# Optimization experiments

Hardware: AMD Instinct MI355X
Metric: run time of the kernel (lower is better)

The kernel has to match this reference:

```python
import jax, jax.numpy as jnp
import numpy as np

B = 32768
T = 1024  # num_time_bins


def setup_inputs() -> dict:
    key = jax.random.key(0)
    k1, k2, k3, k4 = jax.random.split(key, 4)
    hazard_values = jax.random.uniform(k1, (B, T), dtype=jnp.float32)
    labels_Y = jax.random.uniform(k2, (B,), dtype=jnp.float32) * T
    # nn.Linear(T, T): weight [T, T] (out, in), bias [T]
    lim = 1.0 / np.sqrt(T)
    W = jax.random.uniform(k3, (T, T), minval=-lim, maxval=lim, dtype=jnp.float32)
    b = jax.random.uniform(k4, (T,), minval=-lim, maxval=lim, dtype=jnp.float32)
    return {"hazard_values": hazard_values, "labels_Y": labels_Y, "W": W, "b": b}


def reference(hazard_values, labels_Y, W, b):
    # linear + sigmoid + argmax -> per-row truncation position
    logits = hazard_values @ W.T + b                       # [B, T]
    trunc_pos = jnp.argmax(jax.nn.sigmoid(logits), axis=1, keepdims=True)  # [B, 1] int
    # survival curve
    S = jnp.cumprod(1.0 - hazard_values, axis=1)           # [B, T]
    # vectorized truncation decay: for t >= p, multiply by exp(-(t - p))
    t = jnp.arange(T)[None, :]                             # [1, T]
    decay = jnp.where(t >= trunc_pos,
                      jnp.exp(-(t - trunc_pos).astype(S.dtype)),
                      jnp.ones((), S.dtype))
    S = S * decay
    # MSE between argmax position and labels (original prints; we skip prints)
    p = trunc_pos[:, 0].astype(jnp.float32)
    truncation_loss = jnp.mean((p - labels_Y) ** 2)
    return trunc_pos, S, truncation_loss
```

## Files before the change

kernel.cpp:

```cpp
#include <hip/hip_runtime.h>

#define B_ROWS 32768
#define T_BINS 1024

typedef __attribute__((ext_vector_type(8))) _Float16 half8;
typedef __attribute__((ext_vector_type(4))) float floatx4;

__device__ __forceinline__ unsigned long long pack_max(float v, int col) {
    unsigned x = __float_as_uint(v);
    x = (x & 0x80000000u) ? ~x : (x | 0x80000000u);
    return ((unsigned long long)x << 32) | (unsigned)(~col);
}

__device__ __forceinline__ void async16h(const _Float16* g, _Float16* l) {
    __builtin_amdgcn_global_load_lds(
        (const __attribute__((address_space(1))) unsigned int*)g,
        (__attribute__((address_space(3))) unsigned int*)l,
        16, 0, 0);
}

__global__ __launch_bounds__(256) void tof16_kernel(
    const float* __restrict__ src, _Float16* __restrict__ dst, int n4)
{
    int idx = blockIdx.x * 256 + threadIdx.x;
    if (idx >= n4) return;
    float4 x = ((const float4*)src)[idx];
    union { _Float16 h[4]; ushort4 u; } cv;
    cv.h[0] = (_Float16)x.x;
    cv.h[1] = (_Float16)x.y;
    cv.h[2] = (_Float16)x.z;
    cv.h[3] = (_Float16)x.w;
    ((ushort4*)dst)[idx] = cv.u;
}

__global__ __launch_bounds__(256, 2) void mega_kernel(
    const float* __restrict__ A, const _Float16* __restrict__ Wh,
    const float* __restrict__ bias, const float* __restrict__ labels,
    float* __restrict__ out_trunc, float* __restrict__ out_S,
    float* __restrict__ loss_acc)
{
    __shared__ _Float16 sA[2][64 * 64];
    __shared__ _Float16 sW[2][256 * 64];

    const int tid  = threadIdx.x;
    const int lane = tid & 63;
    const int wc   = tid >> 6;
    const int by   = blockIdx.x;

    const int arow = tid >> 2;
    const int ac   = tid & 3;
    const int x8a  = (arow ^ (arow >> 3)) & 7;
    const int sAw0 = arow * 64 + (((ac * 2) ^ x8a) * 8);
    const int sAw1 = arow * 64 + (((ac * 2 + 1) ^ x8a) * 8);
    const float* Abase = A + (size_t)(by * 64 + arow) * T_BINS + ac * 16;

    const int l3   = lane >> 3;
    const int wsl  = lane & 7;

    const int l15  = lane & 15;
    const int hi   = lane >> 4;
    const int xc   = (l15 & 7) ^ (l15 >> 3);

    float run_best[4][4];
    int   run_col[4][4];
#pragma unroll
    for (int i = 0; i < 4; ++i)
#pragma unroll
        for (int r = 0; r < 4; ++r) { run_best[i][r] = -3.4e38f; run_col[i][r] = 0; }

    {
        float4 f0 = *(const float4*)(Abase + 0);
        float4 f1 = *(const float4*)(Abase + 4);
        float4 f2 = *(const float4*)(Abase + 8);
        float4 f3 = *(const float4*)(Abase + 12);
        half8 h0, h1;
        h0[0] = (_Float16)f0.x; h0[1] = (_Float16)f0.y; h0[2] = (_Float16)f0.z; h0[3] = (_Float16)f0.w;
        h0[4] = (_Float16)f1.x; h0[5] = (_Float16)f1.y; h0[6] = (_Float16)f1.z; h0[7] = (_Float16)f1.w;
        h1[0] = (_Float16)f2.x; h1[1] = (_Float16)f2.y; h1[2] = (_Float16)f2.z; h1[3] = (_Float16)f2.w;
        h1[4] = (_Float16)f3.x; h1[5] = (_Float16)f3.y; h1[6] = (_Float16)f3.z; h1[7] = (_Float16)f3.w;
        *(half8*)&sA[0][sAw0] = h0;
        *(half8*)&sA[0][sAw1] = h1;
    }
#pragma unroll
    for (int r = 0; r < 8; ++r)
        async16h(Wh + (size_t)(wc * 64 + r * 8 + l3) * T_BINS + ((wsl ^ l3 ^ r) * 8),
                 &sW[0][(wc * 64 + r * 8) * 64]);
    float4 pa0 = *(const float4*)(Abase + 64);
    float4 pa1 = *(const float4*)(Abase + 68);
    float4 pa2 = *(const float4*)(Abase + 72);
    float4 pa3 = *(const float4*)(Abase + 76);
    __syncthreads();

    int n = 0;
    for (int bx = 0; bx < 4; ++bx) {
        const int colbase = bx * 256 + wc * 64 + l15;
        float bj[4];
#pragma unroll
        for (int j = 0; j < 4; ++j) bj[j] = bias[colbase + j * 16];

        floatx4 acc[4][4];
#pragma unroll
        for (int i = 0; i < 4; ++i)
#pragma unroll
            for (int j = 0; j < 4; ++j) acc[i][j] = (floatx4){0.f, 0.f, 0.f, 0.f};

        for (int t = 0; t < 16; ++t, ++n) {
            const int cur = n & 1;
            const int nxt = cur ^ 1;

            if (n < 63) {
                const int m   = n + 1;
                const int bxn = m >> 4;
                const int k0n = (m & 15) * 64;

#pragma unroll
                for (int r = 0; r < 8; ++r)
                    async16h(Wh + (size_t)(bxn * 256 + wc * 64 + r * 8 + l3) * T_BINS
                                + k0n + ((wsl ^ l3 ^ r) * 8),
                             &sW[nxt][(wc * 64 + r * 8) * 64]);

                const int kq = ((n + 2) & 15) * 64;
                float4 qa0 = *(const float4*)(Abase + kq + 0);
                float4 qa1 = *(const float4*)(Abase + kq + 4);
                float4 qa2 = *(const float4*)(Abase + kq + 8);
                float4 qa3 = *(const float4*)(Abase + kq + 12);

                {
                    half8 h0, h1;
                    h0[0] = (_Float16)pa0.x; h0[1] = (_Float16)pa0.y; h0[2] = (_Float16)pa0.z; h0[3] = (_Float16)pa0.w;
                    h0[4] = (_Float16)pa1.x; h0[5] = (_Float16)pa1.y; h0[6] = (_Float16)pa1.z; h0[7] = (_Float16)pa1.w;
                    h1[0] = (_Float16)pa2.x; h1[1] = (_Float16)pa2.y; h1[2] = (_Float16)pa2.z; h1[3] = (_Float16)pa2.w;
                    h1[4] = (_Float16)pa3.x; h1[5] = (_Float16)pa3.y; h1[6] = (_Float16)pa3.z; h1[7] = (_Float16)pa3.w;
                    *(half8*)&sA[nxt][sAw0] = h0;
                    *(half8*)&sA[nxt][sAw1] = h1;
                }
                pa0 = qa0; pa1 = qa1; pa2 = qa2; pa3 = qa3;
            }

#pragma unroll
            for (int g = 0; g < 2; ++g) {
                half8 ah[4], whf[4];
#pragma unroll
                for (int i = 0; i < 4; ++i)
                    ah[i] = *(const half8*)&sA[cur][(i * 16 + l15) * 64
                                                    + (((g * 4 + hi) ^ xc ^ (i * 2)) * 8)];
#pragma unroll
                for (int j = 0; j < 4; ++j)
                    whf[j] = *(const half8*)&sW[cur][(wc * 64 + j * 16 + l15) * 64
                                                     + (((g * 4 + hi) ^ xc ^ (j * 2)) * 8)];
#pragma unroll
                for (int i = 0; i < 4; ++i)
#pragma unroll
                    for (int j = 0; j < 4; ++j)
                        acc[i][j] = __builtin_amdgcn_mfma_f32_16x16x32_f16(ah[i], whf[j], acc[i][j], 0, 0, 0);
            }

            __syncthreads();
        }

#pragma unroll
        for (int i = 0; i < 4; ++i)
#pragma unroll
            for (int r = 0; r < 4; ++r)
#pragma unroll
                for (int j = 0; j < 4; ++j) {
                    float v = acc[i][j][r] + bj[j];
                    if (v > run_best[i][r]) { run_best[i][r] = v; run_col[i][r] = colbase + j * 16; }
                }
    }

    unsigned long long (*cand)[64] = reinterpret_cast<unsigned long long (*)[64]>(&sA[0][0]);
    float* trunc_s = reinterpret_cast<float*>(&sA[0][0]) + 512;

#pragma unroll
    for (int i = 0; i < 4; ++i)
#pragma unroll
        for (int r = 0; r < 4; ++r) {
            float best = run_best[i][r];
            int   bc   = run_col[i][r];
#pragma unroll
            for (int off = 8; off >= 1; off >>= 1) {
                float ov = __shfl_xor(best, off, 64);
                int   oc = __shfl_xor(bc, off, 64);
                if (ov > best || (ov == best && oc < bc)) { best = ov; bc = oc; }
            }
            if ((lane & 15) == 0)
                cand[wc][i * 16 + (lane >> 4) * 4 + r] = pack_max(best, bc);
        }
    __syncthreads();

    if (tid < 64) {
        unsigned long long m01 = cand[0][tid] > cand[1][tid] ? cand[0][tid] : cand[1][tid];
        unsigned long long m23 = cand[2][tid] > cand[3][tid] ? cand[2][tid] : cand[3][tid];
        unsigned long long mm = m01 > m23 ? m01 : m23;
        unsigned col = ~(unsigned)mm;
        float p = (float)col;
        int rowG = by * 64 + tid;
        out_trunc[rowG] = p;
        trunc_s[tid] = p;
        float d = p - labels[rowG];
        float term = d * d * (1.0f / (float)B_ROWS);
#pragma unroll
        for (int off = 32; off >= 1; off >>= 1)
            term += __shfl_down(term, off, 64);
        if (tid == 0) atomicAdd(loss_acc, term);
    }
    __syncthreads();

    for (int rr = 0; rr < 16; ++rr) {
        int row  = wc * 16 + rr;
        int rowG = by * 64 + row;
        const float* Hrow = A + (size_t)rowG * T_BINS + lane * 16;
        float4 h0 = *(const float4*)(Hrow + 0);
        float4 h1 = *(const float4*)(Hrow + 4);
        float4 h2 = *(const float4*)(Hrow + 8);
        float4 h3 = *(const float4*)(Hrow + 12);
        float hv[16] = {h0.x, h0.y, h0.z, h0.w, h1.x, h1.y, h1.z, h1.w,
                        h2.x, h2.y, h2.z, h2.w, h3.x, h3.y, h3.z, h3.w};
        float vprod[16];
        float run = 1.f;
#pragma unroll
        for (int j = 0; j < 16; ++j) { run *= (1.f - hv[j]); vprod[j] = run; }
        float x = run;
#pragma unroll
        for (int off = 1; off < 64; off <<= 1) {
            float o = __shfl_up(x, off, 64);
            if (lane >= off) x *= o;
        }
        float pre = __shfl_up(x, 1, 64);
        if (lane == 0) pre = 1.f;

        int p  = (int)trunc_s[row];
        int t0 = lane * 16;
        float sv[16];
#pragma unroll
        for (int j = 0; j < 16; ++j) {
            float s = pre * vprod[j];
            int t = t0 + j;
            if (t >= p) s *= __expf((float)(p - t));
            sv[j] = s;
        }
        float* Srow = out_S + (size_t)rowG * T_BINS + lane * 16;
        *(float4*)(Srow + 0)  = (float4){sv[0],  sv[1],  sv[2],  sv[3]};
        *(float4*)(Srow + 4)  = (float4){sv[4],  sv[5],  sv[6],  sv[7]};
        *(float4*)(Srow + 8)  = (float4){sv[8],  sv[9],  sv[10], sv[11]};
        *(float4*)(Srow + 12) = (float4){sv[12], sv[13], sv[14], sv[15]};
    }
}

#define BMf 64
#define BKf 16
#define LDSS (BMf + 4)
__global__ __launch_bounds__(256) void gemm_argmax_fp32(
    const float* __restrict__ A, const float* __restrict__ W,
    const float* __restrict__ bias, unsigned long long* __restrict__ rec)
{
    __shared__ float As[BKf][LDSS];
    __shared__ float Ws[BKf][LDSS];
    const int tid = threadIdx.x;
    const int tx = tid & 15, ty = tid >> 4;
    const int bx = blockIdx.x, by = blockIdx.y;
    const int ar = tid >> 2, ak = (tid & 3) << 2;
    const float* Arow = A + (size_t)(by * BMf + ar) * T_BINS + ak;
    const float* Wrow = W + (size_t)(bx * BMf + ar) * T_BINS + ak;
    float acc[4][4];
#pragma unroll
    for (int i = 0; i < 4; ++i)
#pragma unroll
        for (int j = 0; j < 4; ++j) acc[i][j] = 0.f;
    for (int k0 = 0; k0 < T_BINS; k0 += BKf) {
        float4 av = *(const float4*)(Arow + k0);
        float4 wvv = *(const float4*)(Wrow + k0);
        As[ak + 0][ar] = av.x; As[ak + 1][ar] = av.y; As[ak + 2][ar] = av.z; As[ak + 3][ar] = av.w;
        Ws[ak + 0][ar] = wvv.x; Ws[ak + 1][ar] = wvv.y; Ws[ak + 2][ar] = wvv.z; Ws[ak + 3][ar] = wvv.w;
        __syncthreads();
#pragma unroll
        for (int k = 0; k < BKf; ++k) {
            float4 a4 = *(const float4*)&As[k][ty * 4];
            float4 w4 = *(const float4*)&Ws[k][tx * 4];
            float aa[4] = {a4.x, a4.y, a4.z, a4.w};
            float ww[4] = {w4.x, w4.y, w4.z, w4.w};
#pragma unroll
            for (int i = 0; i < 4; ++i)
#pragma unroll
                for (int j = 0; j < 4; ++j) acc[i][j] = fmaf(aa[i], ww[j], acc[i][j]);
        }
        __syncthreads();
    }
    const int colBase = bx * BMf + tx * 4;
    float bv[4];
#pragma unroll
    for (int j = 0; j < 4; ++j) bv[j] = bias[colBase + j];
#pragma unroll
    for (int i = 0; i < 4; ++i) {
        float best = acc[i][0] + bv[0];
        int bc = colBase;
#pragma unroll
        for (int j = 1; j < 4; ++j) {
            float v = acc[i][j] + bv[j];
            if (v > best) { best = v; bc = colBase + j; }
        }
#pragma unroll
        for (int off = 8; off >= 1; off >>= 1) {
            float ov = __shfl_xor(best, off, 64);
            int oc = __shfl_xor(bc, off, 64);
            if (ov > best || (ov == best && oc < bc)) { best = ov; bc = oc; }
        }
        if (tx == 0) atomicMax(&rec[by * BMf + ty * 4 + i], pack_max(best, bc));
    }
}

__global__ __launch_bounds__(256) void finalize_kernel(
    const unsigned long long* __restrict__ rec, const float* __restrict__ labels,
    float* __restrict__ out_trunc, float* __restrict__ loss_acc)
{
    int i = blockIdx.x * 256 + threadIdx.x;
    unsigned col = ~(unsigned)(rec[i] & 0xFFFFFFFFull);
    float p = (float)col;
    out_trunc[i] = p;
    float d = p - labels[i];
    float term = d * d * (1.0f / (float)B_ROWS);
#pragma unroll
    for (int off = 32; off >= 1; off >>= 1)
        term += __shfl_down(term, off, 64);
    __shared__ float partials[4];
    int lane = threadIdx.x & 63, wv = threadIdx.x >> 6;
    if (lane == 0) partials[wv] = term;
    __syncthreads();
    if (threadIdx.x == 0)
        atomicAdd(loss_acc, partials[0] + partials[1] + partials[2] + partials[3]);
}

__global__ __launch_bounds__(256) void scan_kernel_f32(
    const float* __restrict__ H, const float* __restrict__ trunc_f,
    float* __restrict__ Sout)
{
    const int row = blockIdx.x;
    const int tid = threadIdx.x;
    const int lane = tid & 63;
    const int wv = tid >> 6;
    const float4 h = *(const float4*)(H + (size_t)row * T_BINS + tid * 4);
    float l0 = 1.f - h.x;
    float l1 = l0 * (1.f - h.y);
    float l2 = l1 * (1.f - h.z);
    float l3 = l2 * (1.f - h.w);
    float x = l3;
#pragma unroll
    for (int off = 1; off < 64; off <<= 1) {
        float o = __shfl_up(x, off, 64);
        if (lane >= off) x *= o;
    }
    float ex = __shfl_up(x, 1, 64);
    if (lane == 0) ex = 1.f;
    __shared__ float wtot[4];
    if (lane == 63) wtot[wv] = x;
    __syncthreads();
    float wpre = 1.f;
#pragma unroll
    for (int w = 0; w < 3; ++w)
        if (w < wv) wpre *= wtot[w];
    float pre = wpre * ex;
    int p = (int)trunc_f[row];
    int t0 = tid * 4;
    float sv[4] = {pre * l0, pre * l1, pre * l2, pre * l3};
#pragma unroll
    for (int j = 0; j < 4; ++j) {
        int t = t0 + j;
        if (t >= p) sv[j] *= __expf((float)(p - t));
    }
    float4 s4 = {sv[0], sv[1], sv[2], sv[3]};
    *(float4*)(Sout + (size_t)row * T_BINS + tid * 4) = s4;
}

extern "C" void kernel_launch(void* const* d_in, const int* in_sizes, int n_in,
                              void* d_out, int out_size, void* d_ws, size_t ws_size,
                              hipStream_t stream)
{
    const float* hazard = (const float*)d_in[0];
    const float* labels = (const float*)d_in[1];
    const float* W      = (const float*)d_in[2];
    const float* bias   = (const float*)d_in[3];

    float* out       = (float*)d_out;
    float* out_trunc = out;
    float* out_S     = out + B_ROWS;
    float* out_loss  = out + B_ROWS + (size_t)B_ROWS * T_BINS;

    hipMemsetAsync(out_loss, 0, sizeof(float), stream);

    const size_t NW = (size_t)T_BINS * T_BINS;
    if (ws_size >= NW * sizeof(_Float16)) {
        _Float16* Wh = (_Float16*)d_ws;
        tof16_kernel<<<(int)(NW / 4 / 256), 256, 0, stream>>>(W, Wh, (int)(NW / 4));
        mega_kernel<<<B_ROWS / 64, 256, 0, stream>>>(
            hazard, Wh, bias, labels, out_trunc, out_S, out_loss);
    } else {
        unsigned long long* rec = (unsigned long long*)out_S;
        hipMemsetAsync(rec, 0, (size_t)B_ROWS * sizeof(unsigned long long), stream);
        dim3 ggrid(T_BINS / BMf, B_ROWS / BMf);
        gemm_argmax_fp32<<<ggrid, 256, 0, stream>>>(hazard, W, bias, rec);
        finalize_kernel<<<B_ROWS / 256, 256, 0, stream>>>(rec, labels, out_trunc, out_loss);
        scan_kernel_f32<<<B_ROWS, 256, 0, stream>>>(hazard, out_trunc, out_S);
    }
}
```

Measured before the change: 354.1 us.

## Split mega kernel work across 8 waves per block instead of 4

Doubles the block to 512 threads so each wave computes a 64x32 output sub-tile instead of 64x64. The A and W staging loads are redistributed across the 8 waves, with the swizzle adjusted by an extra per-wave XOR term. The argmax candidate merge now reduces over 8 waves, and the scan/decay epilogue handles 8 rows per wave. The aim is more waves in flight and fewer accumulator registers per thread to hide latency, at the cost of re-reading the A fragments from LDS twice as often per MFMA.

```diff
diff --git a/kernel.cpp b/kernel.cpp
--- a/kernel.cpp
+++ b/kernel.cpp
@@ -33,7 +33,7 @@
     ((ushort4*)dst)[idx] = cv.u;
 }
 
-__global__ __launch_bounds__(256, 2) void mega_kernel(
+__global__ __launch_bounds__(512, 4) void mega_kernel(
     const float* __restrict__ A, const _Float16* __restrict__ Wh,
     const float* __restrict__ bias, const float* __restrict__ labels,
     float* __restrict__ out_trunc, float* __restrict__ out_S,
@@ -44,22 +44,23 @@
 
     const int tid  = threadIdx.x;
     const int lane = tid & 63;
-    const int wc   = tid >> 6;
+    const int w    = tid >> 6;
     const int by   = blockIdx.x;
 
-    const int arow = tid >> 2;
-    const int ac   = tid & 3;
+    const int arow = tid >> 3;
+    const int c8   = tid & 7;
     const int x8a  = (arow ^ (arow >> 3)) & 7;
-    const int sAw0 = arow * 64 + (((ac * 2) ^ x8a) * 8);
-    const int sAw1 = arow * 64 + (((ac * 2 + 1) ^ x8a) * 8);
-    const float* Abase = A + (size_t)(by * 64 + arow) * T_BINS + ac * 16;
-
-    const int l3   = lane >> 3;
-    const int wsl  = lane & 7;
-
-    const int l15  = lane & 15;
-    const int hi   = lane >> 4;
-    const int xc   = (l15 & 7) ^ (l15 >> 3);
+    const int asc  = c8 ^ x8a;
+    const float* Abase = A + (size_t)(by * 64 + arow) * T_BINS + asc * 8;
+    const int sAw  = arow * 64 + c8 * 8;
+
+    const int l3  = lane >> 3;
+    const int wsl = lane & 7;
+    const int w4  = (w & 1) * 4;
+
+    const int l15 = lane & 15;
+    const int hi  = lane >> 4;
+    const int xc  = (l15 & 7) ^ (l15 >> 3);
 
     float run_best[4][4];
     int   run_col[4][4];
@@ -71,38 +72,31 @@
     {
         float4 f0 = *(const float4*)(Abase + 0);
         float4 f1 = *(const float4*)(Abase + 4);
-        float4 f2 = *(const float4*)(Abase + 8);
-        float4 f3 = *(const float4*)(Abase + 12);
-        half8 h0, h1;
-        h0[0] = (_Float16)f0.x; h0[1] = (_Float16)f0.y; h0[2] = (_Float16)f0.z; h0[3] = (_Float16)f0.w;
-        h0[4] = (_Float16)f1.x; h0[5] = (_Float16)f1.y; h0[6] = (_Float16)f1.z; h0[7] = (_Float16)f1.w;
-        h1[0] = (_Float16)f2.x; h1[1] = (_Float16)f2.y; h1[2] = (_Float16)f2.z; h1[3] = (_Float16)f2.w;
-        h1[4] = (_Float16)f3.x; h1[5] = (_Float16)f3.y; h1[6] = (_Float16)f3.z; h1[7] = (_Float16)f3.w;
-        *(half8*)&sA[0][sAw0] = h0;
-        *(half8*)&sA[0][sAw1] = h1;
-    }
-#pragma unroll
-    for (int r = 0; r < 8; ++r)
-        async16h(Wh + (size_t)(wc * 64 + r * 8 + l3) * T_BINS + ((wsl ^ l3 ^ r) * 8),
-                 &sW[0][(wc * 64 + r * 8) * 64]);
+        half8 hv;
+        hv[0] = (_Float16)f0.x; hv[1] = (_Float16)f0.y; hv[2] = (_Float16)f0.z; hv[3] = (_Float16)f0.w;
+        hv[4] = (_Float16)f1.x; hv[5] = (_Float16)f1.y; hv[6] = (_Float16)f1.z; hv[7] = (_Float16)f1.w;
+        *(half8*)&sA[0][sAw] = hv;
+    }
+#pragma unroll
+    for (int r = 0; r < 4; ++r)
+        async16h(Wh + (size_t)(w * 32 + r * 8 + l3) * T_BINS + ((wsl ^ l3 ^ w4 ^ r) * 8),
+                 &sW[0][(w * 32 + r * 8) * 64]);
     float4 pa0 = *(const float4*)(Abase + 64);
     float4 pa1 = *(const float4*)(Abase + 68);
-    float4 pa2 = *(const float4*)(Abase + 72);
-    float4 pa3 = *(const float4*)(Abase + 76);
     __syncthreads();
 
     int n = 0;
     for (int bx = 0; bx < 4; ++bx) {
-        const int colbase = bx * 256 + wc * 64 + l15;
-        float bj[4];
-#pragma unroll
-        for (int j = 0; j < 4; ++j) bj[j] = bias[colbase + j * 16];
-
-        floatx4 acc[4][4];
+        const int colbase = bx * 256 + w * 32 + l15;
+        float bj[2];
+        bj[0] = bias[colbase];
+        bj[1] = bias[colbase + 16];
+
+        floatx4 acc[4][2];
 #pragma unroll
         for (int i = 0; i < 4; ++i)
 #pragma unroll
-            for (int j = 0; j < 4; ++j) acc[i][j] = (floatx4){0.f, 0.f, 0.f, 0.f};
+            for (int j = 0; j < 2; ++j) acc[i][j] = (floatx4){0.f, 0.f, 0.f, 0.f};
 
         for (int t = 0; t < 16; ++t, ++n) {
             const int cur = n & 1;
@@ -114,44 +108,41 @@
                 const int k0n = (m & 15) * 64;
 
 #pragma unroll
-                for (int r = 0; r < 8; ++r)
-                    async16h(Wh + (size_t)(bxn * 256 + wc * 64 + r * 8 + l3) * T_BINS
-                                + k0n + ((wsl ^ l3 ^ r) * 8),
-                             &sW[nxt][(wc * 64 + r * 8) * 64]);
+                for (int r = 0; r < 4; ++r)
+                    async16h(Wh + (size_t)(bxn * 256 + w * 32 + r * 8 + l3) * T_BINS
+                                + k0n + ((wsl ^ l3 ^ w4 ^ r) * 8),
+                             &sW[nxt][(w * 32 + r * 8) * 64]);
 
                 const int kq = ((n + 2) & 15) * 64;
                 float4 qa0 = *(const float4*)(Abase + kq + 0);
                 float4 qa1 = *(const float4*)(Abase + kq + 4);
-                float4 qa2 = *(const float4*)(Abase + kq + 8);
-                float4 qa3 = *(const float4*)(Abase + kq + 12);
 
                 {
-                    half8 h0, h1;
-                    h0[0] = (_Float16)pa0.x; h0[1] = (_Float16)pa0.y; h0[2] = (_Float16)pa0.z; h0[3] = (_Float16)pa0.w;
-                    h0[4] = (_Float16)pa1.x; h0[5] = (_Float16)pa1.y; h0[6] = (_Float16)pa1.z; h0[7] = (_Float16)pa1.w;
-                    h1[0] = (_Float16)pa2.x; h1[1] = (_Float16)pa2.y; h1[2] = (_Float16)pa2.z; h1[3] = (_Float16)pa2.w;
-                    h1[4] = (_Float16)pa3.x; h1[5] = (_Float16)pa3.y; h1[6] = (_Float16)pa3.z; h1[7] = (_Float16)pa3.w;
-                    *(half8*)&sA[nxt][sAw0] = h0;
-                    *(half8*)&sA[nxt][sAw1] = h1;
+                    half8 hv;
+                    hv[0] = (_Float16)pa0.x; hv[1] = (_Float16)pa0.y;
+                    hv[2] = (_Float16)pa0.z; hv[3] = (_Float16)pa0.w;
+                    hv[4] = (_Float16)pa1.x; hv[5] = (_Float16)pa1.y;
+                    hv[6] = (_Float16)pa1.z; hv[7] = (_Float16)pa1.w;
+                    *(half8*)&sA[nxt][sAw] = hv;
                 }
-                pa0 = qa0; pa1 = qa1; pa2 = qa2; pa3 = qa3;
+                pa0 = qa0; pa1 = qa1;
             }
 
 #pragma unroll
             for (int g = 0; g < 2; ++g) {
-                half8 ah[4], whf[4];
+                half8 ah[4], whf[2];
 #pragma unroll
                 for (int i = 0; i < 4; ++i)
                     ah[i] = *(const half8*)&sA[cur][(i * 16 + l15) * 64
                                                     + (((g * 4 + hi) ^ xc ^ (i * 2)) * 8)];
 #pragma unroll
-                for (int j = 0; j < 4; ++j)
-                    whf[j] = *(const half8*)&sW[cur][(wc * 64 + j * 16 + l15) * 64
-                                                     + (((g * 4 + hi) ^ xc ^ (j * 2)) * 8)];
+                for (int j = 0; j < 2; ++j)
+                    whf[j] = *(const half8*)&sW[cur][(w * 32 + j * 16 + l15) * 64
+                                                     + (((g * 4 + hi) ^ xc ^ (j * 2) ^ w4) * 8)];
 #pragma unroll
                 for (int i = 0; i < 4; ++i)
 #pragma unroll
-                    for (int j = 0; j < 4; ++j)
+                    for (int j = 0; j < 2; ++j)
                         acc[i][j] = __builtin_amdgcn_mfma_f32_16x16x32_f16(ah[i], whf[j], acc[i][j], 0, 0, 0);
             }
 
@@ -163,14 +154,14 @@
 #pragma unroll
             for (int r = 0; r < 4; ++r)
 #pragma unroll
-                for (int j = 0; j < 4; ++j) {
+                for (int j = 0; j < 2; ++j) {
                     float v = acc[i][j][r] + bj[j];
                     if (v > run_best[i][r]) { run_best[i][r] = v; run_col[i][r] = colbase + j * 16; }
                 }
     }
 
     unsigned long long (*cand)[64] = reinterpret_cast<unsigned long long (*)[64]>(&sA[0][0]);
-    float* trunc_s = reinterpret_cast<float*>(&sA[0][0]) + 512;
+    float* trunc_s = reinterpret_cast<float*>(&sA[0][0]) + 1024;
 
 #pragma unroll
     for (int i = 0; i < 4; ++i)
@@ -184,15 +175,19 @@
                 int   oc = __shfl_xor(bc, off, 64);
                 if (ov > best || (ov == best && oc < bc)) { best = ov; bc = oc; }
             }
-            if ((lane & 15) == 0)
-                cand[wc][i * 16 + (lane >> 4) * 4 + r] = pack_max(best, bc);
+            if (l15 == 0)
+                cand[w][i * 16 + hi * 4 + r] = pack_max(best, bc);
         }
     __syncthreads();
 
     if (tid < 64) {
         unsigned long long m01 = cand[0][tid] > cand[1][tid] ? cand[0][tid] : cand[1][tid];
         unsigned long long m23 = cand[2][tid] > cand[3][tid] ? cand[2][tid] : cand[3][tid];
-        unsigned long long mm = m01 > m23 ? m01 : m23;
+        unsigned long long m45 = cand[4][tid] > cand[5][tid] ? cand[4][tid] : cand[5][tid];
+        unsigned long long m67 = cand[6][tid] > cand[7][tid] ? cand[6][tid] : cand[7][tid];
+        unsigned long long ma  = m01 > m23 ? m01 : m23;
+        unsigned long long mb  = m45 > m67 ? m45 : m67;
+        unsigned long long mm  = ma > mb ? ma : mb;
         unsigned col = ~(unsigned)mm;
         float p = (float)col;
         int rowG = by * 64 + tid;
@@ -207,8 +202,8 @@
     }
     __syncthreads();
 
-    for (int rr = 0; rr < 16; ++rr) {
-        int row  = wc * 16 + rr;
+    for (int rr = 0; rr < 8; ++rr) {
+        int row  = w * 8 + rr;
         int rowG = by * 64 + row;
         const float* Hrow = A + (size_t)rowG * T_BINS + lane * 16;
         float4 h0 = *(const float4*)(Hrow + 0);
@@ -392,7 +387,7 @@
     if (ws_size >= NW * sizeof(_Float16)) {
         _Float16* Wh = (_Float16*)d_ws;
         tof16_kernel<<<(int)(NW / 4 / 256), 256, 0, stream>>>(W, Wh, (int)(NW / 4));
-        mega_kernel<<<B_ROWS / 64, 256, 0, stream>>>(
+        mega_kernel<<<B_ROWS / 64, 512, 0, stream>>>(
             hazard, Wh, bias, labels, out_trunc, out_S, out_loss);
     } else {
         unsigned long long* rec = (unsigned long long*)out_S;
```

Result: faster. 347.0 us (median of 2 runs) (-2.0%).
